# Kernel optimization log

Measured on AMD Instinct MI355X. Metric: run time of the kernel, lower is better.

Reference implementation:

```python
import jax, jax.numpy as jnp
import numpy as np

D_MODEL = 1024
D_STATE = 16
D_CONV = 4
EXPAND = 2
D_INNER = EXPAND * D_MODEL          # 2048
DT_RANK = (D_MODEL + 15) // 16      # 64
BATCH = 2
SEQLEN = 2048


def setup_inputs() -> dict:
    key = jax.random.key(0)
    ks = jax.random.split(key, 10)

    def rn(k, shape, scale=0.02):
        return (jax.random.normal(k, shape, jnp.float32) * scale).astype(jnp.float32)

    x = jax.random.normal(ks[0], (BATCH, SEQLEN, D_MODEL), jnp.float32)
    W_in = rn(ks[1], (2 * D_INNER, D_MODEL))
    conv_w = rn(ks[2], (D_INNER, D_CONV), 0.1)
    conv_b = jnp.zeros((D_INNER,), jnp.float32)
    W_x = rn(ks[3], (DT_RANK + 2 * D_STATE, D_INNER))
    dt_std = DT_RANK ** -0.5
    W_dt = jax.random.uniform(ks[4], (D_INNER, DT_RANK), jnp.float32, -dt_std, dt_std)
    # dt bias init: inverse softplus of dt ~ LogUniform(1e-3, 1e-1)
    dt = jnp.exp(jax.random.uniform(ks[5], (D_INNER,), jnp.float32)
                 * (np.log(0.1) - np.log(0.001)) + np.log(0.001))
    dt = jnp.clip(dt, 1e-4, None)
    b_dt = dt + jnp.log(-jnp.expm1(-dt))
    # A_log = log(1..d_state) broadcast over d_inner (S4D-real init)
    A_log = jnp.log(jnp.tile(jnp.arange(1, D_STATE + 1, dtype=jnp.float32)[None, :],
                             (D_INNER, 1)))
    Dp = jnp.ones((D_INNER,), jnp.float32)
    W_out1 = rn(ks[6], (D_INNER, 2 * D_INNER))
    W_out2 = rn(ks[7], (D_MODEL, D_INNER))
    return {"x": x, "W_in": W_in, "conv_w": conv_w, "conv_b": conv_b,
            "W_x": W_x, "W_dt": W_dt, "b_dt": b_dt, "A_log": A_log,
            "Dp": Dp, "W_out1": W_out1, "W_out2": W_out2}


def _mefi_forward(x, W_in, conv_w, conv_b, W_x, W_dt, b_dt, A_log, Dp, W_out1, W_out2):
    B, L, _ = x.shape
    # in_proj: (b,l,d) -> (b, 2*d_inner, l)
    xz = jnp.einsum('bld,ed->bel', x, W_in)
    xi, z = xz[:, :D_INNER, :], xz[:, D_INNER:, :]

    # causal depthwise conv1d (left pad d_conv-1) + SiLU
    xc = jax.lax.conv_general_dilated(
        xi, conv_w[:, None, :], window_strides=(1,), padding=[(D_CONV - 1, 0)],
        dimension_numbers=('NCH', 'OIH', 'NCH'), feature_group_count=D_INNER)
    u = jax.nn.silu(xc + conv_b[None, :, None])  # (b, d_inner, l)

    # x_proj -> dt / B / C
    x_dbl = jnp.einsum('bdl,ed->ble', u, W_x)           # (b, l, dt_rank+2n)
    dt_r = x_dbl[..., :DT_RANK]                          # (b, l, r)
    Bm = x_dbl[..., DT_RANK:DT_RANK + D_STATE].transpose(0, 2, 1)  # (b, n, l)
    Cm = x_dbl[..., DT_RANK + D_STATE:].transpose(0, 2, 1)          # (b, n, l)
    dt = jnp.einsum('blr,dr->bdl', dt_r, W_dt)           # (b, d_inner, l)

    A = -jnp.exp(A_log)                                  # (d_inner, n)
    delta = jax.nn.softplus(dt + b_dt[None, :, None])    # (b, d_inner, l)

    # selective scan over time
    def step(s, inp):
        d_t, u_t, B_t, C_t = inp  # (b,d) (b,d) (b,n) (b,n)
        dA = jnp.exp(d_t[:, :, None] * A[None, :, :])
        s = dA * s + (d_t * u_t)[:, :, None] * B_t[:, None, :]
        y_t = jnp.einsum('bdn,bn->bd', s, C_t)
        return s, y_t

    s0 = jnp.zeros((B, D_INNER, D_STATE), delta.dtype)
    xs = (delta.transpose(2, 0, 1), u.transpose(2, 0, 1),
          Bm.transpose(2, 0, 1), Cm.transpose(2, 0, 1))
    _, ys = jax.lax.scan(step, s0, xs)                   # (l, b, d)
    y = ys.transpose(1, 2, 0)                            # (b, d, l)
    y = (y + Dp[None, :, None] * u) * jax.nn.silu(z)     # gated scan output

    # interaction term: tr_term = C^T @ S_t^T (S_t == A), plus D @ x
    y_t = jnp.einsum('bnl,dn->bld', Cm, A) \
        + jnp.einsum('d,bdl->bl', Dp, u)[..., None]      # (b, l, d_inner)

    # cat along channels then out_proj MLP
    y_cat = jnp.concatenate([y.transpose(0, 2, 1), y_t], axis=-1)  # (b, l, 2*d_inner)
    h = jnp.maximum(y_cat @ W_out1.T, 0.0)
    return h @ W_out2.T                                   # (b, l, d_model)


def reference(x, W_in, conv_w, conv_b, W_x, W_dt, b_dt, A_log, Dp, W_out1, W_out2):
    return _mefi_forward(x, W_in, conv_w, conv_b, W_x, W_dt, b_dt, A_log, Dp, W_out1, W_out2)
```

## Files before the change

kernel.cpp:

```cpp
#include <hip/hip_runtime.h>
#include <hip/hip_bf16.h>
#include <math.h>

#define D_MODEL 1024
#define D_STATE 16
#define D_INNER 2048
#define DT_RANK 64
#define BATCH   2
#define SEQLEN  2048
#define NPROJ   96
#define XSTR    128
#define NCHUNK  16
#define CHUNK   128
#define XKS     8

typedef __attribute__((ext_vector_type(8))) __bf16 bf16x8;
typedef __attribute__((ext_vector_type(4))) float f32x4;

__device__ __forceinline__ float silu_f(float x) { return x / (1.f + __expf(-x)); }

__device__ __forceinline__ void gload_lds16(const void* g, void* l) {
    __builtin_amdgcn_global_load_lds((const __attribute__((address_space(1))) void*)g,
                                     (__attribute__((address_space(3))) void*)l, 16, 0, 0);
}

template<int RELU, int OUT_BF16>
__global__ __launch_bounds__(256) void gemm_bf16_k(
    const __bf16* __restrict__ A, const __bf16* __restrict__ B, void* __restrict__ Cv,
    int K, int lda, int ldb, int ldc, long long sA, long long sB, long long sC)
{
    __shared__ alignas(16) __bf16 As[128 * 32];
    __shared__ alignas(16) __bf16 Bs[128 * 32];
    const int bz = blockIdx.z;
    A += (long long)bz * sA;
    B += (long long)bz * sB;
    int nwg = gridDim.x * gridDim.y;
    int flat = blockIdx.y * gridDim.x + blockIdx.x;
    int swz = (nwg & 7) ? flat : ((flat & 7) * (nwg >> 3) + (flat >> 3));
    const int m0 = (swz / gridDim.x) * 128, n0 = (swz % gridDim.x) * 128;
    const int tid = threadIdx.x;
    const int lane = tid & 63;
    const int wv = tid >> 6;
    const int wr = wv >> 1, wc = wv & 1;

    f32x4 acc[4][4];
    #pragma unroll
    for (int i = 0; i < 4; ++i)
        #pragma unroll
        for (int j = 0; j < 4; ++j) acc[i][j] = (f32x4){0.f, 0.f, 0.f, 0.f};

    const int ko = (lane >> 4) * 8;
    const int fr = lane & 15;

    for (int k0 = 0; k0 < K; k0 += 32) {
        #pragma unroll
        for (int q = 0; q < 2; ++q) {
            int f = tid + q * 256;
            int row = f >> 2, c16 = f & 3;
            gload_lds16(A + (long long)(m0 + row) * lda + k0 + c16 * 8, As + f * 8);
            gload_lds16(B + (long long)(n0 + row) * ldb + k0 + c16 * 8, Bs + f * 8);
        }
        __syncthreads();
        bf16x8 a[4], b[4];
        #pragma unroll
        for (int i = 0; i < 4; ++i) {
            a[i] = *(const bf16x8*)(As + (wr * 64 + i * 16 + fr) * 32 + ko);
            b[i] = *(const bf16x8*)(Bs + (wc * 64 + i * 16 + fr) * 32 + ko);
        }
        #pragma unroll
        for (int i = 0; i < 4; ++i)
            #pragma unroll
            for (int j = 0; j < 4; ++j)
                acc[i][j] = __builtin_amdgcn_mfma_f32_16x16x32_bf16(a[i], b[j], acc[i][j], 0, 0, 0);
        __syncthreads();
    }

    #pragma unroll
    for (int i = 0; i < 4; ++i) {
        const int row = m0 + wr * 64 + i * 16 + (lane >> 4) * 4;
        #pragma unroll
        for (int j = 0; j < 4; ++j) {
            const int col = n0 + wc * 64 + j * 16 + fr;
            #pragma unroll
            for (int r = 0; r < 4; ++r) {
                float v = acc[i][j][r];
                if (RELU) v = fmaxf(v, 0.f);
                if (OUT_BF16)
                    ((__bf16*)Cv)[(long long)bz * sC + (long long)(row + r) * ldc + col] = (__bf16)v;
                else
                    ((float*)Cv)[(long long)bz * sC + (long long)(row + r) * ldc + col] = v;
            }
        }
    }
}

__global__ void cvt_bf16_k(const float* __restrict__ in, __bf16* __restrict__ out, int n8) {
    int i = blockIdx.x * 256 + threadIdx.x;
    if (i >= n8) return;
    const f32x4* p = (const f32x4*)in + (long long)i * 2;
    f32x4 v0 = p[0], v1 = p[1];
    bf16x8 o;
    o[0] = (__bf16)v0[0]; o[1] = (__bf16)v0[1]; o[2] = (__bf16)v0[2]; o[3] = (__bf16)v0[3];
    o[4] = (__bf16)v1[0]; o[5] = (__bf16)v1[1]; o[6] = (__bf16)v1[2]; o[7] = (__bf16)v1[3];
    ((bf16x8*)out)[i] = o;
}

template<int SOFTPLUS>
__global__ __launch_bounds__(256) void gemm_nt_k(
    const float* __restrict__ A, const float* __restrict__ B, float* __restrict__ C,
    const float* __restrict__ bias,
    int M, int N, int K, int lda, int ldb, int ldc,
    long long sA, long long sB, long long sC)
{
    __shared__ float As[16][68];
    __shared__ float Bs[16][68];
    const int bz = blockIdx.z;
    A += (long long)bz * sA; B += (long long)bz * sB; C += (long long)bz * sC;
    const int m0 = blockIdx.y * 64, n0 = blockIdx.x * 64;
    const int tid = threadIdx.x;
    const int lk = tid & 15, lr = tid >> 4;
    const int tx = tid & 15, ty = tid >> 4;
    float acc[4][4] = {};
    for (int k0 = 0; k0 < K; k0 += 16) {
        #pragma unroll
        for (int q = 0; q < 4; ++q) {
            int i = lr + q * 16;
            As[lk][i] = A[(long long)(m0 + i) * lda + k0 + lk];
            Bs[lk][i] = B[(long long)(n0 + i) * ldb + k0 + lk];
        }
        __syncthreads();
        #pragma unroll
        for (int k = 0; k < 16; ++k) {
            float a[4], b[4];
            #pragma unroll
            for (int j = 0; j < 4; ++j) { a[j] = As[k][ty*4+j]; b[j] = Bs[k][tx*4+j]; }
            #pragma unroll
            for (int i = 0; i < 4; ++i)
                #pragma unroll
                for (int j = 0; j < 4; ++j) acc[i][j] += a[i] * b[j];
        }
        __syncthreads();
    }
    #pragma unroll
    for (int i = 0; i < 4; ++i) {
        const int m = m0 + ty * 4 + i;
        float bi = SOFTPLUS ? bias[m] : 0.f;
        #pragma unroll
        for (int j = 0; j < 4; ++j) {
            float v = acc[i][j];
            if (SOFTPLUS) {
                v += bi;
                v = fmaxf(v, 0.f) + log1pf(expf(-fabsf(v)));
            }
            C[(long long)m * ldc + n0 + tx*4 + j] = v;
        }
    }
}

__global__ void aneg_k(const float* __restrict__ A_log, float* __restrict__ Aneg) {
    int i = blockIdx.x * 256 + threadIdx.x;
    if (i < D_INNER * D_STATE) Aneg[i] = -expf(A_log[i]);
}

__global__ __launch_bounds__(256) void conv_silu_k(const float* __restrict__ xz,
    const float* __restrict__ cw, const float* __restrict__ cb,
    float* __restrict__ u, __bf16* __restrict__ ut)
{
    __shared__ float tile[32][33];
    const int b = blockIdx.z;
    const int d0 = blockIdx.y * 32, l0 = blockIdx.x * 32;
    const int lx = threadIdx.x, dy = threadIdx.y;
    #pragma unroll
    for (int j = 0; j < 4; ++j) {
        int d = d0 + dy + j * 8;
        const float* xi = xz + ((long long)b * 2 * D_INNER + d) * SEQLEN;
        int l = l0 + lx;
        float acc = cb[d];
        #pragma unroll
        for (int k = 0; k < 4; ++k) {
            int t = l + k - 3;
            if (t >= 0) acc += xi[t] * cw[d * 4 + k];
        }
        float v = silu_f(acc);
        u[((long long)b * D_INNER + d) * SEQLEN + l] = v;
        tile[dy + j * 8][lx] = v;
    }
    __syncthreads();
    #pragma unroll
    for (int j = 0; j < 4; ++j) {
        int l = l0 + dy + j * 8;
        ut[((long long)b * SEQLEN + l) * D_INNER + d0 + lx] = (__bf16)tile[lx][dy + j * 8];
    }
}

__global__ void xdbl_red_k(const float* __restrict__ xpart, float* __restrict__ xdbl) {
    int i = blockIdx.x * 256 + threadIdx.x;
    const f32x4* p = (const f32x4*)xpart;
    f32x4 s = p[i];
    #pragma unroll
    for (int ks = 1; ks < XKS; ++ks) {
        f32x4 v = p[(long long)ks * (BATCH * SEQLEN * XSTR / 4) + i];
        s.x += v.x; s.y += v.y; s.z += v.z; s.w += v.w;
    }
    ((f32x4*)xdbl)[i] = s;
}

__global__ __launch_bounds__(64, 1) void scan_p1_k(const float* __restrict__ delta,
    const float* __restrict__ u, const float* __restrict__ xdbl,
    const float* __restrict__ Aneg, float* __restrict__ chA, float* __restrict__ chS)
{
    const int q = threadIdx.x >> 4;
    const int n = threadIdx.x & 15;
    const int gg = blockIdx.x * 4 + q;
    const int g = gg >> 4, c = gg & (NCHUNK - 1);
    const int b = g >> 11, d = g & (D_INNER - 1);
    const float a = Aneg[d * D_STATE + n];
    const long long base = (long long)g * SEQLEN + c * CHUNK;
    const float4* dv = (const float4*)(delta + base);
    const float4* uv = (const float4*)(u + base);
    const float* xb = xdbl + ((long long)b * SEQLEN + c * CHUNK) * XSTR + DT_RANK + n;

    float4 pd[4], pu[4];
    float pB[16];
    #pragma unroll
    for (int i = 0; i < 4; ++i) { pd[i] = dv[i]; pu[i] = uv[i]; }
    #pragma unroll
    for (int i = 0; i < 16; ++i) pB[i] = xb[i * XSTR];

    float s = 0.f, ap = 1.f;
    for (int t0 = 0; t0 < CHUNK; t0 += 16) {
        float cd[16], cu[16], cB[16];
        #pragma unroll
        for (int i = 0; i < 4; ++i) {
            cd[4*i] = pd[i].x; cd[4*i+1] = pd[i].y; cd[4*i+2] = pd[i].z; cd[4*i+3] = pd[i].w;
            cu[4*i] = pu[i].x; cu[4*i+1] = pu[i].y; cu[4*i+2] = pu[i].z; cu[4*i+3] = pu[i].w;
        }
        #pragma unroll
        for (int i = 0; i < 16; ++i) cB[i] = pB[i];
        if (t0 + 16 < CHUNK) {
            const int nb = (t0 >> 2) + 4;
            #pragma unroll
            for (int i = 0; i < 4; ++i) { pd[i] = dv[nb + i]; pu[i] = uv[nb + i]; }
            const float* xn = xb + (t0 + 16) * XSTR;
            #pragma unroll
            for (int i = 0; i < 16; ++i) pB[i] = xn[i * XSTR];
        }
        float dA[16], wB[16];
        #pragma unroll
        for (int i = 0; i < 16; ++i) {
            dA[i] = __expf(cd[i] * a);
            wB[i] = cd[i] * cu[i] * cB[i];
        }
        #pragma unroll
        for (int i = 0; i < 16; ++i) {
            s = dA[i] * s + wB[i];
            ap *= dA[i];
        }
    }
    chA[(long long)gg * 16 + n] = ap;
    chS[(long long)gg * 16 + n] = s;
}

__global__ void scan_comb_k(const float* __restrict__ chA, const float* __restrict__ chS,
                            float* __restrict__ sinit)
{
    int idx = blockIdx.x * 256 + threadIdx.x;
    int g = idx >> 4, n = idx & 15;
    const float* A = chA + (long long)g * (NCHUNK * 16) + n;
    const float* S = chS + (long long)g * (NCHUNK * 16) + n;
    float av[NCHUNK], sv[NCHUNK];
    #pragma unroll
    for (int c = 0; c < NCHUNK; ++c) { av[c] = A[c * 16]; sv[c] = S[c * 16]; }
    float* si = sinit + (long long)g * (NCHUNK * 16) + n;
    float carry = 0.f;
    #pragma unroll
    for (int c = 0; c < NCHUNK; ++c) {
        si[c * 16] = carry;
        carry = sv[c] + av[c] * carry;
    }
}

__global__ __launch_bounds__(64, 1) void scan_p3_k(const float* __restrict__ delta,
    const float* __restrict__ u, const float* __restrict__ xdbl,
    const float* __restrict__ Aneg, const float* __restrict__ sinit, float* __restrict__ y)
{
    __shared__ float lp[4][16][17];
    const int q = threadIdx.x >> 4;
    const int n = threadIdx.x & 15;
    const int gg = blockIdx.x * 4 + q;
    const int g = gg >> 4, c = gg & (NCHUNK - 1);
    const int b = g >> 11, d = g & (D_INNER - 1);
    const float a = Aneg[d * D_STATE + n];
    const long long base = (long long)g * SEQLEN + c * CHUNK;
    const float4* dv = (const float4*)(delta + base);
    const float4* uv = (const float4*)(u + base);
    const float* xb = xdbl + ((long long)b * SEQLEN + c * CHUNK) * XSTR + DT_RANK + n;
    float* yl = y + base;

    float4 pd[4], pu[4];
    float pB[16], pC[16];
    #pragma unroll
    for (int i = 0; i < 4; ++i) { pd[i] = dv[i]; pu[i] = uv[i]; }
    #pragma unroll
    for (int i = 0; i < 16; ++i) { pB[i] = xb[i * XSTR]; pC[i] = xb[i * XSTR + D_STATE]; }

    float s = sinit[(long long)gg * 16 + n];
    for (int t0 = 0; t0 < CHUNK; t0 += 16) {
        float cd[16], cu[16], cB[16], cC[16];
        #pragma unroll
        for (int i = 0; i < 4; ++i) {
            cd[4*i] = pd[i].x; cd[4*i+1] = pd[i].y; cd[4*i+2] = pd[i].z; cd[4*i+3] = pd[i].w;
            cu[4*i] = pu[i].x; cu[4*i+1] = pu[i].y; cu[4*i+2] = pu[i].z; cu[4*i+3] = pu[i].w;
        }
        #pragma unroll
        for (int i = 0; i < 16; ++i) { cB[i] = pB[i]; cC[i] = pC[i]; }
        if (t0 + 16 < CHUNK) {
            const int nb = (t0 >> 2) + 4;
            #pragma unroll
            for (int i = 0; i < 4; ++i) { pd[i] = dv[nb + i]; pu[i] = uv[nb + i]; }
            const float* xn = xb + (t0 + 16) * XSTR;
            #pragma unroll
            for (int i = 0; i < 16; ++i) { pB[i] = xn[i * XSTR]; pC[i] = xn[i * XSTR + D_STATE]; }
        }
        float dA[16], wB[16];
        #pragma unroll
        for (int i = 0; i < 16; ++i) {
            dA[i] = __expf(cd[i] * a);
            wB[i] = cd[i] * cu[i] * cB[i];
        }
        #pragma unroll
        for (int i = 0; i < 16; ++i) {
            s = dA[i] * s + wB[i];
            lp[q][n][i] = s * cC[i];
        }
        __syncthreads();
        float v[16];
        #pragma unroll
        for (int j = 0; j < 16; ++j) v[j] = lp[q][j][n];
        float acc = 0.f;
        #pragma unroll
        for (int j = 0; j < 16; ++j) acc += v[j];
        yl[t0 + n] = acc;
        __syncthreads();
    }
}

__global__ void ssum_k(const float* __restrict__ u, const float* __restrict__ Dp,
                       float* __restrict__ S)
{
    int li = blockIdx.x * 256 + threadIdx.x;
    int c = blockIdx.y;
    int b = li >> 11, l = li & (SEQLEN - 1);
    const float* up = u + (long long)b * D_INNER * SEQLEN + l;
    float acc = 0.f;
    for (int d = c * 256; d < c * 256 + 256; ++d)
        acc += Dp[d] * up[(long long)d * SEQLEN];
    atomicAdd(&S[li], acc);
}

__global__ __launch_bounds__(256) void ytrans_k(const float* __restrict__ ysc,
    const float* __restrict__ u, const float* __restrict__ xz,
    const float* __restrict__ Dp, __bf16* __restrict__ ycat)
{
    __shared__ float tile[32][33];
    const int b = blockIdx.z;
    const int d0 = blockIdx.y * 32, l0 = blockIdx.x * 32;
    const int lx = threadIdx.x, dy = threadIdx.y;
    #pragma unroll
    for (int j = 0; j < 4; ++j) {
        int d = d0 + dy + j * 8;
        long long i  = ((long long)b * D_INNER + d) * SEQLEN + l0 + lx;
        long long iz = ((long long)b * 2 * D_INNER + D_INNER + d) * SEQLEN + l0 + lx;
        tile[dy + j * 8][lx] = (ysc[i] + Dp[d] * u[i]) * silu_f(xz[iz]);
    }
    __syncthreads();
    #pragma unroll
    for (int j = 0; j < 4; ++j) {
        int l = l0 + dy + j * 8;
        ycat[((long long)b * SEQLEN + l) * (2 * D_INNER) + d0 + lx] = (__bf16)tile[lx][dy + j * 8];
    }
}

__global__ __launch_bounds__(256) void yt_k(const float* __restrict__ xdbl,
    const float* __restrict__ Aneg, const float* __restrict__ S, __bf16* __restrict__ ycat)
{
    __shared__ float Cs[16][33];
    __shared__ float An[16][64];
    __shared__ float Sv[32];
    const int b = blockIdx.z;
    const int d0 = blockIdx.y * 64, l0 = blockIdx.x * 32;
    const int tid = threadIdx.x;
    for (int f = tid; f < 512; f += 256) {
        int n = f & 15, l = f >> 4;
        Cs[n][l] = xdbl[((long long)b * SEQLEN + l0 + l) * XSTR + DT_RANK + D_STATE + n];
    }
    for (int f = tid; f < 1024; f += 256) {
        int n = f & 15, d = f >> 4;
        An[n][d] = Aneg[(d0 + d) * D_STATE + n];
    }
    if (tid < 32) Sv[tid] = S[b * SEQLEN + l0 + tid];
    __syncthreads();
    const int dx = tid & 63, lg = tid >> 6;
    #pragma unroll
    for (int j = 0; j < 8; ++j) {
        int l = lg * 8 + j;
        float acc = Sv[l];
        #pragma unroll
        for (int n = 0; n < 16; ++n) acc += Cs[n][l] * An[n][dx];
        ycat[((long long)b * SEQLEN + l0 + l) * (2 * D_INNER) + D_INNER + d0 + dx] = (__bf16)acc;
    }
}

extern "C" void kernel_launch(void* const* d_in, const int* in_sizes, int n_in,
                              void* d_out, int out_size, void* d_ws, size_t ws_size,
                              hipStream_t stream)
{
    const float* x      = (const float*)d_in[0];
    const float* W_in   = (const float*)d_in[1];
    const float* conv_w = (const float*)d_in[2];
    const float* conv_b = (const float*)d_in[3];
    const float* W_x    = (const float*)d_in[4];
    const float* W_dt   = (const float*)d_in[5];
    const float* b_dt   = (const float*)d_in[6];
    const float* A_log  = (const float*)d_in[7];
    const float* Dp     = (const float*)d_in[8];
    const float* W_out1 = (const float*)d_in[9];
    const float* W_out2 = (const float*)d_in[10];
    float* out = (float*)d_out;
    float* ws  = (float*)d_ws;

    float* xz    = ws;
    float* u     = xz    + 16777216;
    float* xdblp = u     + 8388608;
    float* dtb   = xdblp + 524288;
    float* ysc   = dtb   + 8388608;
    float* Aneg  = ysc   + 8388608;
    float* S     = Aneg  + 32768;
    __bf16* ycat16 = (__bf16*)(S + 4096);
    __bf16* h16    = ycat16 + 16777216;
    __bf16* W_in16  = (__bf16*)u;
    __bf16* xb16    = W_in16 + 4194304;
    __bf16* Wout116 = (__bf16*)dtb;
    __bf16* Wout216 = Wout116 + 8388608;
    __bf16* ut16  = ycat16;
    float* chA    = (float*)(ut16 + 8388608);
    float* chS    = chA + 1048576;
    float* sinitb = chS + 1048576;
    __bf16* Wx16p = h16;
    float* xpart  = dtb;

    hipMemsetAsync(S, 0, 4096 * sizeof(float), stream);
    aneg_k<<<128, 256, 0, stream>>>(A_log, Aneg);

    cvt_bf16_k<<<2048, 256, 0, stream>>>(W_in, W_in16, 524288);
    cvt_bf16_k<<<2048, 256, 0, stream>>>(x, xb16, 524288);
    cvt_bf16_k<<<96, 256, 0, stream>>>(W_x, Wx16p, 24576);
    hipMemsetAsync(Wx16p + 96 * D_INNER, 0, 32 * D_INNER * sizeof(__bf16), stream);

    gemm_bf16_k<0, 0><<<dim3(16, 32, BATCH), 256, 0, stream>>>(
        W_in16, xb16, xz, D_MODEL, D_MODEL, D_MODEL, SEQLEN,
        0LL, (long long)SEQLEN * D_MODEL, (long long)4096 * SEQLEN);

    conv_silu_k<<<dim3(SEQLEN / 32, D_INNER / 32, BATCH), dim3(32, 8), 0, stream>>>(
        xz, conv_w, conv_b, u, ut16);

    gemm_bf16_k<0, 0><<<dim3(1, 32, XKS), 256, 0, stream>>>(
        ut16, Wx16p, xpart, D_INNER / XKS, D_INNER, D_INNER, XSTR,
        (long long)(D_INNER / XKS), (long long)(D_INNER / XKS),
        (long long)BATCH * SEQLEN * XSTR);
    xdbl_red_k<<<(BATCH * SEQLEN * XSTR / 4) / 256, 256, 0, stream>>>(xpart, xdblp);

    gemm_nt_k<1><<<dim3(SEQLEN / 64, D_INNER / 64, BATCH), 256, 0, stream>>>(
        W_dt, xdblp, dtb, b_dt, D_INNER, SEQLEN, DT_RANK, DT_RANK, XSTR, SEQLEN,
        0LL, (long long)SEQLEN * XSTR, (long long)D_INNER * SEQLEN);

    scan_p1_k<<<(BATCH * D_INNER * NCHUNK) / 4, 64, 0, stream>>>(dtb, u, xdblp, Aneg, chA, chS);
    scan_comb_k<<<256, 256, 0, stream>>>(chA, chS, sinitb);
    scan_p3_k<<<(BATCH * D_INNER * NCHUNK) / 4, 64, 0, stream>>>(dtb, u, xdblp, Aneg, sinitb, ysc);

    cvt_bf16_k<<<4096, 256, 0, stream>>>(W_out1, Wout116, 1048576);
    cvt_bf16_k<<<1024, 256, 0, stream>>>(W_out2, Wout216, 262144);

    ssum_k<<<dim3((BATCH * SEQLEN) / 256, 8), 256, 0, stream>>>(u, Dp, S);

    ytrans_k<<<dim3(SEQLEN / 32, D_INNER / 32, BATCH), dim3(32, 8), 0, stream>>>(ysc, u, xz, Dp, ycat16);

    yt_k<<<dim3(SEQLEN / 32, D_INNER / 64, BATCH), 256, 0, stream>>>(xdblp, Aneg, S, ycat16);

    gemm_bf16_k<1, 1><<<dim3(16, 32, 1), 256, 0, stream>>>(
        ycat16, Wout116, h16, 2 * D_INNER, 2 * D_INNER, 2 * D_INNER, D_INNER,
        0LL, 0LL, 0LL);

    gemm_bf16_k<0, 0><<<dim3(8, 32, 1), 256, 0, stream>>>(
        h16, Wout216, out, D_INNER, D_INNER, D_INNER, D_MODEL,
        0LL, 0LL, 0LL);
}
```

Measured before the change: 556.4 us.

## Fuse chunked scan passes and carry combine into one block per channel

The three scan kernels (per-chunk state reduction, cross-chunk carry combine, chunk replay with output) become one kernel with one 256-thread block per (batch, channel), so all 16 chunks live in one block. Chunk carries are exchanged through shared memory instead of global chA/chS/sinit buffers, which removes two kernel launches and that global traffic. In exchange, the carry combine runs serially on 16 threads while the rest of the block waits at a barrier, and the larger block with heavier shared memory use may change occupancy.

```diff
diff --git a/kernel.cpp b/kernel.cpp
--- a/kernel.cpp
+++ b/kernel.cpp
@@ -205,14 +205,17 @@
     ((f32x4*)xdbl)[i] = s;
 }
 
-__global__ __launch_bounds__(64, 1) void scan_p1_k(const float* __restrict__ delta,
+__global__ __launch_bounds__(256, 1) void scan_f_k(const float* __restrict__ delta,
     const float* __restrict__ u, const float* __restrict__ xdbl,
-    const float* __restrict__ Aneg, float* __restrict__ chA, float* __restrict__ chS)
-{
-    const int q = threadIdx.x >> 4;
-    const int n = threadIdx.x & 15;
-    const int gg = blockIdx.x * 4 + q;
-    const int g = gg >> 4, c = gg & (NCHUNK - 1);
+    const float* __restrict__ Aneg, float* __restrict__ y)
+{
+    __shared__ float combA[NCHUNK][16];
+    __shared__ float combS[NCHUNK][16];
+    __shared__ float sins[NCHUNK][16];
+    __shared__ float lp[NCHUNK][16][17];
+    const int tid = threadIdx.x;
+    const int c = tid >> 4, n = tid & 15;
+    const int g = blockIdx.x;
     const int b = g >> 11, d = g & (D_INNER - 1);
     const float a = Aneg[d * D_STATE + n];
     const long long base = (long long)g * SEQLEN + c * CHUNK;
@@ -257,54 +260,31 @@
             ap *= dA[i];
         }
     }
-    chA[(long long)gg * 16 + n] = ap;
-    chS[(long long)gg * 16 + n] = s;
-}
-
-__global__ void scan_comb_k(const float* __restrict__ chA, const float* __restrict__ chS,
-                            float* __restrict__ sinit)
-{
-    int idx = blockIdx.x * 256 + threadIdx.x;
-    int g = idx >> 4, n = idx & 15;
-    const float* A = chA + (long long)g * (NCHUNK * 16) + n;
-    const float* S = chS + (long long)g * (NCHUNK * 16) + n;
-    float av[NCHUNK], sv[NCHUNK];
-    #pragma unroll
-    for (int c = 0; c < NCHUNK; ++c) { av[c] = A[c * 16]; sv[c] = S[c * 16]; }
-    float* si = sinit + (long long)g * (NCHUNK * 16) + n;
-    float carry = 0.f;
-    #pragma unroll
-    for (int c = 0; c < NCHUNK; ++c) {
-        si[c * 16] = carry;
-        carry = sv[c] + av[c] * carry;
-    }
-}
-
-__global__ __launch_bounds__(64, 1) void scan_p3_k(const float* __restrict__ delta,
-    const float* __restrict__ u, const float* __restrict__ xdbl,
-    const float* __restrict__ Aneg, const float* __restrict__ sinit, float* __restrict__ y)
-{
-    __shared__ float lp[4][16][17];
-    const int q = threadIdx.x >> 4;
-    const int n = threadIdx.x & 15;
-    const int gg = blockIdx.x * 4 + q;
-    const int g = gg >> 4, c = gg & (NCHUNK - 1);
-    const int b = g >> 11, d = g & (D_INNER - 1);
-    const float a = Aneg[d * D_STATE + n];
-    const long long base = (long long)g * SEQLEN + c * CHUNK;
-    const float4* dv = (const float4*)(delta + base);
-    const float4* uv = (const float4*)(u + base);
-    const float* xb = xdbl + ((long long)b * SEQLEN + c * CHUNK) * XSTR + DT_RANK + n;
+    combA[c][n] = ap;
+    combS[c][n] = s;
+    __syncthreads();
+
+    if (c == 0) {
+        float av[NCHUNK], sv[NCHUNK];
+        #pragma unroll
+        for (int cc = 0; cc < NCHUNK; ++cc) { av[cc] = combA[cc][n]; sv[cc] = combS[cc][n]; }
+        float carry = 0.f;
+        #pragma unroll
+        for (int cc = 0; cc < NCHUNK; ++cc) {
+            sins[cc][n] = carry;
+            carry = sv[cc] + av[cc] * carry;
+        }
+    }
+    __syncthreads();
+
     float* yl = y + base;
-
-    float4 pd[4], pu[4];
-    float pB[16], pC[16];
+    float pC[16];
     #pragma unroll
     for (int i = 0; i < 4; ++i) { pd[i] = dv[i]; pu[i] = uv[i]; }
     #pragma unroll
     for (int i = 0; i < 16; ++i) { pB[i] = xb[i * XSTR]; pC[i] = xb[i * XSTR + D_STATE]; }
 
-    float s = sinit[(long long)gg * 16 + n];
+    s = sins[c][n];
     for (int t0 = 0; t0 < CHUNK; t0 += 16) {
         float cd[16], cu[16], cB[16], cC[16];
         #pragma unroll
@@ -331,12 +311,12 @@
         #pragma unroll
         for (int i = 0; i < 16; ++i) {
             s = dA[i] * s + wB[i];
-            lp[q][n][i] = s * cC[i];
+            lp[c][n][i] = s * cC[i];
         }
         __syncthreads();
         float v[16];
         #pragma unroll
-        for (int j = 0; j < 16; ++j) v[j] = lp[q][j][n];
+        for (int j = 0; j < 16; ++j) v[j] = lp[c][j][n];
         float acc = 0.f;
         #pragma unroll
         for (int j = 0; j < 16; ++j) acc += v[j];
@@ -443,9 +423,6 @@
     __bf16* Wout116 = (__bf16*)dtb;
     __bf16* Wout216 = Wout116 + 8388608;
     __bf16* ut16  = ycat16;
-    float* chA    = (float*)(ut16 + 8388608);
-    float* chS    = chA + 1048576;
-    float* sinitb = chS + 1048576;
     __bf16* Wx16p = h16;
     float* xpart  = dtb;
 
@@ -474,9 +451,7 @@
         W_dt, xdblp, dtb, b_dt, D_INNER, SEQLEN, DT_RANK, DT_RANK, XSTR, SEQLEN,
         0LL, (long long)SEQLEN * XSTR, (long long)D_INNER * SEQLEN);
 
-    scan_p1_k<<<(BATCH * D_INNER * NCHUNK) / 4, 64, 0, stream>>>(dtb, u, xdblp, Aneg, chA, chS);
-    scan_comb_k<<<256, 256, 0, stream>>>(chA, chS, sinitb);
-    scan_p3_k<<<(BATCH * D_INNER * NCHUNK) / 4, 64, 0, stream>>>(dtb, u, xdblp, Aneg, sinitb, ysc);
+    scan_f_k<<<BATCH * D_INNER, 256, 0, stream>>>(dtb, u, xdblp, Aneg, ysc);
 
     cvt_bf16_k<<<4096, 256, 0, stream>>>(W_out1, Wout116, 1048576);
     cvt_bf16_k<<<1024, 256, 0, stream>>>(W_out2, Wout216, 262144);
```

Result: faster. 544.4 us (-2.2%).
